# Optimization experiments

Measured on AMD Instinct MI355X. Metric: run time of the kernel, lower is better.

## Reference

```python
import jax, jax.numpy as jnp
import numpy as np

N_NODES = 100000
N_EDGES = 1600000
IN_CH, MID_CH, BOT_CH = 128, 128, 64


def setup_inputs() -> dict:
    key = jax.random.key(0)
    ks = jax.random.split(key, 10)
    x = jax.random.normal(ks[0], (N_NODES, IN_CH), dtype=jnp.float32)
    edge_index = jax.random.randint(ks[1], (2, N_EDGES), 0, N_NODES, dtype=jnp.int64)
    s = 0.05
    # GCNConv weights follow torch Linear convention: out = x @ W.T + b (bias added post-aggregation)
    W1 = jax.random.normal(ks[2], (MID_CH, IN_CH), dtype=jnp.float32) * s
    b1 = jnp.zeros((MID_CH,), dtype=jnp.float32)
    W2 = jax.random.normal(ks[3], (BOT_CH, MID_CH), dtype=jnp.float32) * s
    b2 = jnp.zeros((BOT_CH,), dtype=jnp.float32)
    W3 = jax.random.normal(ks[4], (MID_CH, BOT_CH), dtype=jnp.float32) * s
    b3 = jnp.zeros((MID_CH,), dtype=jnp.float32)
    W4 = jax.random.normal(ks[5], (IN_CH, MID_CH), dtype=jnp.float32) * s
    b4 = jnp.zeros((IN_CH,), dtype=jnp.float32)
    return {"x": x, "edge_index": edge_index,
            "W1": W1, "b1": b1, "W2": W2, "b2": b2,
            "W3": W3, "b3": b3, "W4": W4, "b4": b4}


def _gcn_conv(x, src, dst, norm, W, b, n):
    # linear transform first (small GEMM), then gather-normalize-scatter
    h = x @ W.T                                   # [N, out]
    msg = h[src] * norm[:, None]                  # [E+N, out] gathered messages
    out = jax.ops.segment_sum(msg, dst, num_segments=n)
    return out + b


def reference(x, edge_index, W1, b1, W2, b2, W3, b3, W4, b4):
    n = N_NODES
    # add self-loops (PyG GCNConv default)
    loop = jnp.arange(n, dtype=edge_index.dtype)
    src = jnp.concatenate([edge_index[0], loop])
    dst = jnp.concatenate([edge_index[1], loop])
    # symmetric degree normalization: deg includes self-loops -> deg >= 1
    deg = jax.ops.segment_sum(jnp.ones_like(dst, dtype=x.dtype), dst, num_segments=n)
    dinv = jax.lax.rsqrt(deg)
    norm = dinv[src] * dinv[dst]                  # [E+N]
    # encoder
    h = jax.nn.relu(_gcn_conv(x, src, dst, norm, W1, b1, n))
    z = _gcn_conv(h, src, dst, norm, W2, b2, n)
    # decoder
    h = jax.nn.relu(_gcn_conv(z, src, dst, norm, W3, b3, n))
    out = _gcn_conv(h, src, dst, norm, W4, b4, n)
    return out
```

## Files before the change

### kernel.cpp

```cpp
#include <hip/hip_runtime.h>

typedef unsigned int u32;
typedef unsigned short u16;
typedef short bf16x4 __attribute__((ext_vector_type(4)));
typedef short bf16x8 __attribute__((ext_vector_type(8)));
typedef float f32x4 __attribute__((ext_vector_type(4)));

__device__ inline u16 f2bf_rne(float f) {
    u32 b = __float_as_uint(f);
    return (u16)((b + 0x7FFFu + ((b >> 16) & 1u)) >> 16);
}
__device__ inline u32 packbf2(float lo, float hi) {
    return (u32)f2bf_rne(lo) | ((u32)f2bf_rne(hi) << 16);
}
__device__ inline float bf2f(u16 h) { return __uint_as_float((u32)h << 16); }
__device__ inline float2 bfpair(u32 q) {
    float2 f;
    f.x = __uint_as_float(q << 16);
    f.y = __uint_as_float(q & 0xFFFF0000u);
    return f;
}

__global__ void k_detect(const int* __restrict__ p, int n_int32, u32* __restrict__ flag) {
    __shared__ int s[256];
    int tid = threadIdx.x;
    int acc = 0;
    int limit = n_int32 < 2048 ? n_int32 : 2048;
    for (int i = 1 + 2 * tid; i < limit; i += 512) acc |= p[i];
    s[tid] = acc;
    __syncthreads();
    for (int o = 128; o > 0; o >>= 1) {
        if (tid < o) s[tid] |= s[tid + o];
        __syncthreads();
    }
    if (tid == 0) *flag = (s[0] == 0) ? 1u : 0u;
}

__global__ void k_convert(const void* __restrict__ p, int n, const u32* __restrict__ flag,
                          int* __restrict__ out) {
    int i = blockIdx.x * blockDim.x + threadIdx.x;
    if (i >= n) return;
    if (*flag) out[i] = (int)((const long long*)p)[i];
    else       out[i] = ((const int*)p)[i];
}

template <int CIN, int COUT>
__global__ void k_wpack(const float* __restrict__ W, u16* __restrict__ Wpk) {
    int i = blockIdx.x * 256 + threadIdx.x;
    if (i >= CIN * COUT) return;
    int o = i / CIN, k = i % CIN;
    int fi = o >> 4, l15 = o & 15;
    int ks = k >> 5, w = k & 31;
    int h = w >> 4, l4 = (w & 15) >> 2, off = w & 3;
    int lane = l4 * 16 + l15;
    int e = h * 4 + off;
    constexpr int KS = CIN / 32;
    Wpk[(size_t)(((fi * KS + ks) * 64 + lane) * 8 + e)] = f2bf_rne(W[i]);
}

__global__ void k_init(u32* __restrict__ deg, u32* __restrict__ cnt, int N) {
    int i = blockIdx.x * blockDim.x + threadIdx.x;
    if (i < N) { deg[i] = 1u; cnt[i] = 0u; }
}

__global__ __launch_bounds__(256) void k_count(const int* __restrict__ dst,
                                               u32* __restrict__ deg, int E, int N) {
    int xcd = blockIdx.x & 7;
    int sub = blockIdx.x >> 3;
    int nsub = gridDim.x >> 3;
    int lo = (int)((long long)N * xcd >> 3);
    int hi = (int)((long long)N * (xcd + 1) >> 3);
    for (int e = sub * 256 + threadIdx.x; e < E; e += nsub * 256) {
        int d = dst[e];
        if (d >= lo && d < hi) atomicAdd(&deg[d], 1u);
    }
}

__global__ void k_dinv(const u32* __restrict__ deg, float* __restrict__ dinv, int N) {
    int i = blockIdx.x * blockDim.x + threadIdx.x;
    if (i < N) dinv[i] = rsqrtf((float)deg[i]);
}

__global__ void k_scan_a(const u32* __restrict__ deg, u32* __restrict__ partial, int N) {
    __shared__ u32 s[256];
    int tid = threadIdx.x;
    int base = blockIdx.x * 1024 + tid * 4;
    u32 sum = 0;
#pragma unroll
    for (int j = 0; j < 4; ++j) {
        int v = base + j;
        sum += (v < N) ? (deg[v] - 1u) : 0u;
    }
    s[tid] = sum;
    __syncthreads();
    for (int o = 128; o > 0; o >>= 1) {
        if (tid < o) s[tid] += s[tid + o];
        __syncthreads();
    }
    if (tid == 0) partial[blockIdx.x] = s[0];
}

__global__ void k_scan_b(u32* __restrict__ partial, int NB, int* __restrict__ row_ptr, int N) {
    __shared__ u32 s[128];
    int tid = threadIdx.x;
    u32 v = (tid < NB) ? partial[tid] : 0u;
    s[tid] = v;
    __syncthreads();
    for (int off = 1; off < 128; off <<= 1) {
        u32 t = (tid >= off) ? s[tid - off] : 0u;
        __syncthreads();
        s[tid] += t;
        __syncthreads();
    }
    if (tid < NB) partial[tid] = s[tid] - v;
    if (tid == 127) row_ptr[N] = (int)s[127];
}

__global__ void k_scan_c(const u32* __restrict__ deg, const u32* __restrict__ partial,
                         int* __restrict__ row_ptr, int N) {
    __shared__ u32 s[256];
    int tid = threadIdx.x;
    int base = blockIdx.x * 1024 + tid * 4;
    u32 vals[4];
    u32 sum = 0;
#pragma unroll
    for (int j = 0; j < 4; ++j) {
        int v = base + j;
        vals[j] = (v < N) ? (deg[v] - 1u) : 0u;
        sum += vals[j];
    }
    s[tid] = sum;
    __syncthreads();
    for (int off = 1; off < 256; off <<= 1) {
        u32 t = (tid >= off) ? s[tid - off] : 0u;
        __syncthreads();
        s[tid] += t;
        __syncthreads();
    }
    u32 run = s[tid] - sum + partial[blockIdx.x];
#pragma unroll
    for (int j = 0; j < 4; ++j) {
        int v = base + j;
        if (v < N) row_ptr[v] = (int)run;
        run += vals[j];
    }
}

__global__ __launch_bounds__(256) void k_fill(const int* __restrict__ src,
                                              const int* __restrict__ dst,
                                              const int* __restrict__ row_ptr,
                                              u32* __restrict__ cnt,
                                              int* __restrict__ col, int E, int N) {
    int xcd = blockIdx.x & 7;
    int sub = blockIdx.x >> 3;
    int nsub = gridDim.x >> 3;
    int lo = (int)((long long)N * xcd >> 3);
    int hi = (int)((long long)N * (xcd + 1) >> 3);
    for (int e = sub * 256 + threadIdx.x; e < E; e += nsub * 256) {
        int d = dst[e];
        if (d >= lo && d < hi) {
            int pos = row_ptr[d] + (int)atomicAdd(&cnt[d], 1u);
            col[pos] = src[e];
        }
    }
}

template <int CIN, int COUT, int MODE, bool IN_F32>
__global__ __launch_bounds__(512, 4) void k_mgemm(const void* __restrict__ Xv,
                                                  const u16* __restrict__ Wpk,
                                                  const float* __restrict__ aux,
                                                  u16* __restrict__ Gout, int N,
                                                  int tiles, int tpb) {
    constexpr int PITCH = CIN + 8;
    constexpr int EPITCH = COUT + 8;
    constexpr int KS = CIN / 32;
    constexpr int NT = COUT / 32;
    constexpr int CHUNKS = COUT / 8;
    __shared__ __align__(16) u16 sX[64 * PITCH];
    __shared__ __align__(16) u16 sE[64 * EPITCH];

    int tid = threadIdx.x, wid = tid >> 6, lane = tid & 63;
    int l15 = lane & 15, l4 = lane >> 4;
    int rg = wid >> 1;
    int cg = wid & 1;

    bf16x8 wfrag[NT][KS];
#pragma unroll
    for (int nt = 0; nt < NT; ++nt) {
        int fi = cg * NT + nt;
#pragma unroll
        for (int ks = 0; ks < KS; ++ks)
            wfrag[nt][ks] = *(const bf16x8*)&Wpk[(size_t)(((fi * KS + ks) * 64 + lane) * 8)];
    }
    float bv[NT];
    if (MODE == 1) {
#pragma unroll
        for (int nt = 0; nt < NT; ++nt) bv[nt] = aux[cg * (COUT / 2) + nt * 16 + l15];
    }

    int t0 = blockIdx.x * tpb;
    int t1 = t0 + tpb; if (t1 > tiles) t1 = tiles;

    for (int t = t0; t < t1; ++t) {
        int rowbase = t * 64;

        if (IN_F32) {
            const float* Xf = (const float*)Xv;
            for (int i = tid * 8; i < 64 * CIN; i += 512 * 8) {
                int r = i / CIN, k = i % CIN;
                int row = rowbase + r;
                if (row >= N) row = N - 1;
                const float4* xp = (const float4*)(Xf + (size_t)row * CIN + k);
                float4 a = xp[0], b = xp[1];
                uint4 pk;
                pk.x = packbf2(a.x, a.y);
                pk.y = packbf2(a.z, a.w);
                pk.z = packbf2(b.x, b.y);
                pk.w = packbf2(b.z, b.w);
                *(uint4*)&sX[r * PITCH + k] = pk;
            }
        } else {
            const u16* Xb = (const u16*)Xv;
            for (int i = tid * 8; i < 64 * CIN; i += 512 * 8) {
                int r = i / CIN, k = i % CIN;
                int row = rowbase + r;
                if (row >= N) row = N - 1;
                *(bf16x8*)&sX[r * PITCH + k] = *(const bf16x8*)&Xb[(size_t)row * CIN + k];
            }
        }
        __syncthreads();

        f32x4 acc[NT];
#pragma unroll
        for (int nt = 0; nt < NT; ++nt) acc[nt] = (f32x4){0.f, 0.f, 0.f, 0.f};

        const u16* xrow = &sX[(rg * 16 + l15) * PITCH + 4 * l4];
#pragma unroll
        for (int ks = 0; ks < KS; ++ks) {
            bf16x4 a0 = *(const bf16x4*)(xrow + ks * 32);
            bf16x4 a1 = *(const bf16x4*)(xrow + ks * 32 + 16);
            bf16x8 av = __builtin_shufflevector(a0, a1, 0, 1, 2, 3, 4, 5, 6, 7);
#pragma unroll
            for (int nt = 0; nt < NT; ++nt)
                acc[nt] = __builtin_amdgcn_mfma_f32_16x16x32_bf16(av, wfrag[nt][ks], acc[nt], 0, 0, 0);
        }

#pragma unroll
        for (int i = 0; i < 4; ++i) {
            int rl = rg * 16 + 4 * l4 + i;
            int row = rowbase + rl;
            int rc = row < N ? row : N - 1;
            float s = (MODE == 0) ? aux[rc] : 0.f;
#pragma unroll
            for (int nt = 0; nt < NT; ++nt) {
                float a = acc[nt][i];
                float o = (MODE == 0) ? a * s : fmaxf(a + bv[nt], 0.f);
                sE[rl * EPITCH + cg * (COUT / 2) + nt * 16 + l15] = f2bf_rne(o);
            }
        }
        __syncthreads();

        for (int a = tid; a < 64 * CHUNKS; a += 512) {
            int rl = a / CHUNKS, ch = a % CHUNKS;
            int row = rowbase + rl;
            if (row < N)
                *(uint4*)&Gout[(size_t)row * COUT + ch * 8] =
                    *(const uint4*)&sE[rl * EPITCH + ch * 8];
        }
    }
}

template <bool OUT_BF16, bool RELU, bool HAS_BIAS>
__global__ __launch_bounds__(256) void k_spmm128(const u32* __restrict__ Gq,
                                                 const int* __restrict__ rp,
                                                 const int* __restrict__ col,
                                                 const float* __restrict__ dinv,
                                                 const float* __restrict__ bias,
                                                 void* __restrict__ Y, int N) {
    int wid = threadIdx.x >> 6, lane = threadIdx.x & 63;
    int v0 = blockIdx.x * 8 + wid * 2;
    if (v0 >= N) return;
    int v1 = v0 + 1;
    bool has1 = (v1 < N);

    float2 acc0 = bfpair(Gq[(size_t)v0 * 64 + lane]);
    int e0 = rp[v0], f0 = rp[v0 + 1];
    float2 acc1 = {0.f, 0.f};
    int e1 = 0, f1 = 0;
    if (has1) {
        acc1 = bfpair(Gq[(size_t)v1 * 64 + lane]);
        e1 = f0; f1 = rp[v1 + 1];
    }

    while (e0 + 8 <= f0 && e1 + 8 <= f1) {
        int u0[8], u1[8];
#pragma unroll
        for (int j = 0; j < 8; ++j) u0[j] = col[e0 + j];
#pragma unroll
        for (int j = 0; j < 8; ++j) u1[j] = col[e1 + j];
        u32 q0[8], q1[8];
#pragma unroll
        for (int j = 0; j < 8; ++j) q0[j] = Gq[(size_t)u0[j] * 64 + lane];
#pragma unroll
        for (int j = 0; j < 8; ++j) q1[j] = Gq[(size_t)u1[j] * 64 + lane];
#pragma unroll
        for (int j = 0; j < 8; ++j) {
            float2 a = bfpair(q0[j]);
            acc0.x += a.x; acc0.y += a.y;
        }
#pragma unroll
        for (int j = 0; j < 8; ++j) {
            float2 a = bfpair(q1[j]);
            acc1.x += a.x; acc1.y += a.y;
        }
        e0 += 8; e1 += 8;
    }
    for (; e0 + 8 <= f0; e0 += 8) {
        int u[8];
#pragma unroll
        for (int j = 0; j < 8; ++j) u[j] = col[e0 + j];
        u32 q[8];
#pragma unroll
        for (int j = 0; j < 8; ++j) q[j] = Gq[(size_t)u[j] * 64 + lane];
#pragma unroll
        for (int j = 0; j < 8; ++j) {
            float2 a = bfpair(q[j]);
            acc0.x += a.x; acc0.y += a.y;
        }
    }
    for (; e1 + 8 <= f1; e1 += 8) {
        int u[8];
#pragma unroll
        for (int j = 0; j < 8; ++j) u[j] = col[e1 + j];
        u32 q[8];
#pragma unroll
        for (int j = 0; j < 8; ++j) q[j] = Gq[(size_t)u[j] * 64 + lane];
#pragma unroll
        for (int j = 0; j < 8; ++j) {
            float2 a = bfpair(q[j]);
            acc1.x += a.x; acc1.y += a.y;
        }
    }
    for (; e0 < f0; ++e0) {
        float2 a = bfpair(Gq[(size_t)col[e0] * 64 + lane]);
        acc0.x += a.x; acc0.y += a.y;
    }
    for (; e1 < f1; ++e1) {
        float2 a = bfpair(Gq[(size_t)col[e1] * 64 + lane]);
        acc1.x += a.x; acc1.y += a.y;
    }

    {
        float s = dinv[v0];
        float rx = acc0.x * s, ry = acc0.y * s;
        if (HAS_BIAS) { rx += bias[2 * lane]; ry += bias[2 * lane + 1]; }
        if (RELU) { rx = fmaxf(rx, 0.f); ry = fmaxf(ry, 0.f); }
        if (OUT_BF16) ((u32*)Y)[(size_t)v0 * 64 + lane] = packbf2(rx, ry);
        else {
            float2 o2; o2.x = rx; o2.y = ry;
            *(float2*)((float*)Y + (size_t)v0 * 128 + 2 * lane) = o2;
        }
    }
    if (has1) {
        float s = dinv[v1];
        float rx = acc1.x * s, ry = acc1.y * s;
        if (HAS_BIAS) { rx += bias[2 * lane]; ry += bias[2 * lane + 1]; }
        if (RELU) { rx = fmaxf(rx, 0.f); ry = fmaxf(ry, 0.f); }
        if (OUT_BF16) ((u32*)Y)[(size_t)v1 * 64 + lane] = packbf2(rx, ry);
        else {
            float2 o2; o2.x = rx; o2.y = ry;
            *(float2*)((float*)Y + (size_t)v1 * 128 + 2 * lane) = o2;
        }
    }
}

template <bool OUT_BF16, bool RELU, bool HAS_BIAS, bool PRESCALE>
__global__ __launch_bounds__(256) void k_spmm64(const u16* __restrict__ G16,
                                                const int* __restrict__ rp,
                                                const int* __restrict__ col,
                                                const float* __restrict__ dinv,
                                                const float* __restrict__ bias,
                                                void* __restrict__ Y, int N) {
    int wid = threadIdx.x >> 6, lane = threadIdx.x & 63;
    int v0 = blockIdx.x * 8 + wid * 2;
    if (v0 >= N) return;
    int v1 = v0 + 1;
    bool has1 = (v1 < N);

    float acc0 = bf2f(G16[(size_t)v0 * 64 + lane]);
    int e0 = rp[v0], f0 = rp[v0 + 1];
    float acc1 = 0.f;
    int e1 = 0, f1 = 0;
    if (has1) {
        acc1 = bf2f(G16[(size_t)v1 * 64 + lane]);
        e1 = f0; f1 = rp[v1 + 1];
    }

    while (e0 + 8 <= f0 && e1 + 8 <= f1) {
        int u0[8], u1[8];
#pragma unroll
        for (int j = 0; j < 8; ++j) u0[j] = col[e0 + j];
#pragma unroll
        for (int j = 0; j < 8; ++j) u1[j] = col[e1 + j];
        u16 g0[8], g1[8];
#pragma unroll
        for (int j = 0; j < 8; ++j) g0[j] = G16[(size_t)u0[j] * 64 + lane];
#pragma unroll
        for (int j = 0; j < 8; ++j) g1[j] = G16[(size_t)u1[j] * 64 + lane];
        acc0 += ((bf2f(g0[0]) + bf2f(g0[1])) + (bf2f(g0[2]) + bf2f(g0[3]))) +
                ((bf2f(g0[4]) + bf2f(g0[5])) + (bf2f(g0[6]) + bf2f(g0[7])));
        acc1 += ((bf2f(g1[0]) + bf2f(g1[1])) + (bf2f(g1[2]) + bf2f(g1[3]))) +
                ((bf2f(g1[4]) + bf2f(g1[5])) + (bf2f(g1[6]) + bf2f(g1[7])));
        e0 += 8; e1 += 8;
    }
    for (; e0 + 8 <= f0; e0 += 8) {
        int u[8];
#pragma unroll
        for (int j = 0; j < 8; ++j) u[j] = col[e0 + j];
        u16 g[8];
#pragma unroll
        for (int j = 0; j < 8; ++j) g[j] = G16[(size_t)u[j] * 64 + lane];
        acc0 += ((bf2f(g[0]) + bf2f(g[1])) + (bf2f(g[2]) + bf2f(g[3]))) +
                ((bf2f(g[4]) + bf2f(g[5])) + (bf2f(g[6]) + bf2f(g[7])));
    }
    for (; e1 + 8 <= f1; e1 += 8) {
        int u[8];
#pragma unroll
        for (int j = 0; j < 8; ++j) u[j] = col[e1 + j];
        u16 g[8];
#pragma unroll
        for (int j = 0; j < 8; ++j) g[j] = G16[(size_t)u[j] * 64 + lane];
        acc1 += ((bf2f(g[0]) + bf2f(g[1])) + (bf2f(g[2]) + bf2f(g[3]))) +
                ((bf2f(g[4]) + bf2f(g[5])) + (bf2f(g[6]) + bf2f(g[7])));
    }
    for (; e0 < f0; ++e0) acc0 += bf2f(G16[(size_t)col[e0] * 64 + lane]);
    for (; e1 < f1; ++e1) acc1 += bf2f(G16[(size_t)col[e1] * 64 + lane]);

    {
        float s = dinv[v0];
        float r = acc0 * s;
        if (HAS_BIAS) r += bias[lane];
        if (RELU) r = fmaxf(r, 0.f);
        if (PRESCALE) r *= s;
        if (OUT_BF16) ((u16*)Y)[(size_t)v0 * 64 + lane] = f2bf_rne(r);
        else          ((float*)Y)[(size_t)v0 * 64 + lane] = r;
    }
    if (has1) {
        float s = dinv[v1];
        float r = acc1 * s;
        if (HAS_BIAS) r += bias[lane];
        if (RELU) r = fmaxf(r, 0.f);
        if (PRESCALE) r *= s;
        if (OUT_BF16) ((u16*)Y)[(size_t)v1 * 64 + lane] = f2bf_rne(r);
        else          ((float*)Y)[(size_t)v1 * 64 + lane] = r;
    }
}

extern "C" void kernel_launch(void* const* d_in, const int* in_sizes, int n_in,
                              void* d_out, int out_size, void* d_ws, size_t ws_size,
                              hipStream_t stream) {
    const float* x  = (const float*)d_in[0];
    const void*  ei = d_in[1];
    const float* W1 = (const float*)d_in[2];
    const float* b1 = (const float*)d_in[3];
    const float* W2 = (const float*)d_in[4];
    const float* b2 = (const float*)d_in[5];
    const float* W3 = (const float*)d_in[6];
    const float* b3 = (const float*)d_in[7];
    const float* W4 = (const float*)d_in[8];
    const float* b4 = (const float*)d_in[9];

    const int N = in_sizes[0] / 128;
    const int E = in_sizes[1] / 2;

    size_t off = 0;
    auto alloc = [&](size_t bytes) -> void* {
        void* p = (char*)d_ws + off;
        off += (bytes + 255) & ~(size_t)255;
        return p;
    };
    u32*   flag    = (u32*)  alloc(4);
    int*   src32   = (int*)  alloc((size_t)E * 4);
    int*   dst32   = (int*)  alloc((size_t)E * 4);
    u32*   deg     = (u32*)  alloc((size_t)N * 4);
    float* dinv    = (float*)alloc((size_t)N * 4);
    int*   row_ptr = (int*)  alloc((size_t)(N + 1) * 4);
    u32*   cnt     = (u32*)  alloc((size_t)N * 4);
    u32*   partial = (u32*)  alloc(256 * 4);
    int*   col     = (int*)  alloc((size_t)E * 4);
    u16*   Wp1     = (u16*)  alloc(128 * 128 * 2);
    u16*   Wp2     = (u16*)  alloc(64 * 128 * 2);
    u16*   Wp3     = (u16*)  alloc(128 * 64 * 2);
    u16*   Wp4     = (u16*)  alloc(128 * 128 * 2);
    u16*   BUF1    = (u16*)  alloc((size_t)N * 128 * 2);
    u16*   BUF2    = (u16*)  alloc((size_t)N * 128 * 2);
    u16*   BUF3    = (u16*)  alloc((size_t)N * 64 * 2);
    u16*   Zbf     = (u16*)d_out;

    const int n2 = 2 * E;
    const int NB = (N + 1023) / 1024;

    k_detect<<<1, 256, 0, stream>>>((const int*)ei, n2, flag);
    k_convert<<<(n2 + 255) / 256, 256, 0, stream>>>(ei, n2, flag, src32);
    int* dstp = src32 + E;
    k_init<<<(N + 255) / 256, 256, 0, stream>>>(deg, cnt, N);
    k_count<<<1024, 256, 0, stream>>>(dstp, deg, E, N);
    k_dinv<<<(N + 255) / 256, 256, 0, stream>>>(deg, dinv, N);
    k_scan_a<<<NB, 256, 0, stream>>>(deg, partial, N);
    k_scan_b<<<1, 128, 0, stream>>>(partial, NB, row_ptr, N);
    k_scan_c<<<NB, 256, 0, stream>>>(deg, partial, row_ptr, N);
    k_fill<<<1024, 256, 0, stream>>>(src32, dstp, row_ptr, cnt, col, E, N);
    (void)dst32;

    k_wpack<128, 128><<<(128 * 128 + 255) / 256, 256, 0, stream>>>(W1, Wp1);
    k_wpack<128, 64><<<(128 * 64 + 255) / 256, 256, 0, stream>>>(W2, Wp2);
    k_wpack<64, 128><<<(64 * 128 + 255) / 256, 256, 0, stream>>>(W3, Wp3);
    k_wpack<128, 128><<<(128 * 128 + 255) / 256, 256, 0, stream>>>(W4, Wp4);

    const int tiles = (N + 63) / 64;
    const int gM = tiles < 512 ? tiles : 512;
    const int tpb = (tiles + gM - 1) / gM;
    const int gS = (N + 7) / 8;

    k_mgemm<128, 128, 0, true><<<gM, 512, 0, stream>>>(x, Wp1, dinv, BUF1, N, tiles, tpb);
    k_spmm128<true, true, true><<<gS, 256, 0, stream>>>((const u32*)BUF1, row_ptr, col, dinv, b1, BUF2, N);

    k_mgemm<128, 64, 0, false><<<gM, 512, 0, stream>>>(BUF2, Wp2, dinv, BUF3, N, tiles, tpb);
    k_spmm64<true, false, true, true><<<gS, 256, 0, stream>>>(BUF3, row_ptr, col, dinv, b2, Zbf, N);

    k_spmm64<true, false, false, false><<<gS, 256, 0, stream>>>(Zbf, row_ptr, col, dinv, b2, BUF1, N);
    k_mgemm<64, 128, 1, false><<<gM, 512, 0, stream>>>(BUF1, Wp3, b3, BUF2, N, tiles, tpb);

    k_mgemm<128, 128, 0, false><<<gM, 512, 0, stream>>>(BUF2, Wp4, dinv, BUF1, N, tiles, tpb);
    k_spmm128<false, false, true><<<gS, 256, 0, stream>>>((const u32*)BUF1, row_ptr, col, dinv, b4, d_out, N);
}
```

Before: 490.2 us.

## Fuse decoder GEMMs, restructure 64-wide SpMM with half-wave edge split, add nontemporal loads

Layer-3 and layer-4 dense transforms are fused into one kernel that keeps the ReLU'd intermediate in shared memory, removing a global round trip of the 128-wide hidden activations. The 64-channel SpMM now processes one node per wave, with each half-wave handling alternate edges through 32-bit paired bf16 loads, then combines the halves with a cross-lane shuffle. Edge index loads and the final fp32 output stores use nontemporal hints to reduce cache pollution. The fused GEMM launches one block per tile, needs about 67KB of shared memory and has no persistent looping, which may limit occupancy.

Result: slower. 532.1 us (+8.5%).

```diff
diff --git a/kernel.cpp b/kernel.cpp
--- a/kernel.cpp
+++ b/kernel.cpp
@@ -5,6 +5,7 @@
 typedef short bf16x4 __attribute__((ext_vector_type(4)));
 typedef short bf16x8 __attribute__((ext_vector_type(8)));
 typedef float f32x4 __attribute__((ext_vector_type(4)));
+typedef float f32x2 __attribute__((ext_vector_type(2)));
 
 __device__ inline u16 f2bf_rne(float f) {
     u32 b = __float_as_uint(f);
@@ -270,6 +271,107 @@
     }
 }
 
+__global__ __launch_bounds__(512, 2) void k_mgemm34(const u16* __restrict__ Xb,
+                                                    const u16* __restrict__ Wp3,
+                                                    const u16* __restrict__ Wp4,
+                                                    const float* __restrict__ b3,
+                                                    const float* __restrict__ dinv,
+                                                    u16* __restrict__ Gout, int N) {
+    constexpr int P1 = 72;
+    constexpr int P2 = 136;
+    __shared__ __align__(16) u16 sW4[128 * 128];
+    __shared__ __align__(16) u16 sBuf[64 * P2];
+    __shared__ __align__(16) u16 sH[64 * P2];
+
+    int tid = threadIdx.x, wid = tid >> 6, lane = tid & 63;
+    int l15 = lane & 15, l4 = lane >> 4;
+    int rg = wid >> 1, cg = wid & 1;
+    int rowbase = blockIdx.x * 64;
+
+    bf16x8 wf3[4][2];
+#pragma unroll
+    for (int nt = 0; nt < 4; ++nt) {
+        int fi = cg * 4 + nt;
+#pragma unroll
+        for (int ks = 0; ks < 2; ++ks)
+            wf3[nt][ks] = *(const bf16x8*)&Wp3[(size_t)(((fi * 2 + ks) * 64 + lane) * 8)];
+    }
+    float bv[4];
+#pragma unroll
+    for (int nt = 0; nt < 4; ++nt) bv[nt] = b3[cg * 64 + nt * 16 + l15];
+
+    for (int i = tid * 8; i < 128 * 128; i += 512 * 8)
+        *(bf16x8*)&sW4[i] = *(const bf16x8*)&Wp4[i];
+
+    for (int i = tid * 8; i < 64 * 64; i += 512 * 8) {
+        int r = i / 64, k = i % 64;
+        int row = rowbase + r;
+        if (row >= N) row = N - 1;
+        *(bf16x8*)&sBuf[r * P1 + k] = *(const bf16x8*)&Xb[(size_t)row * 64 + k];
+    }
+    __syncthreads();
+
+    f32x4 acc[4];
+#pragma unroll
+    for (int nt = 0; nt < 4; ++nt) acc[nt] = (f32x4){0.f, 0.f, 0.f, 0.f};
+    {
+        const u16* xrow = &sBuf[(rg * 16 + l15) * P1 + 4 * l4];
+#pragma unroll
+        for (int ks = 0; ks < 2; ++ks) {
+            bf16x4 a0 = *(const bf16x4*)(xrow + ks * 32);
+            bf16x4 a1 = *(const bf16x4*)(xrow + ks * 32 + 16);
+            bf16x8 av = __builtin_shufflevector(a0, a1, 0, 1, 2, 3, 4, 5, 6, 7);
+#pragma unroll
+            for (int nt = 0; nt < 4; ++nt)
+                acc[nt] = __builtin_amdgcn_mfma_f32_16x16x32_bf16(av, wf3[nt][ks], acc[nt], 0, 0, 0);
+        }
+    }
+#pragma unroll
+    for (int i = 0; i < 4; ++i) {
+        int rl = rg * 16 + 4 * l4 + i;
+#pragma unroll
+        for (int nt = 0; nt < 4; ++nt)
+            sH[rl * P2 + cg * 64 + nt * 16 + l15] = f2bf_rne(fmaxf(acc[nt][i] + bv[nt], 0.f));
+    }
+    __syncthreads();
+
+#pragma unroll
+    for (int nt = 0; nt < 4; ++nt) acc[nt] = (f32x4){0.f, 0.f, 0.f, 0.f};
+    {
+        const u16* xrow = &sH[(rg * 16 + l15) * P2 + 4 * l4];
+#pragma unroll
+        for (int ks = 0; ks < 4; ++ks) {
+            bf16x4 a0 = *(const bf16x4*)(xrow + ks * 32);
+            bf16x4 a1 = *(const bf16x4*)(xrow + ks * 32 + 16);
+            bf16x8 av = __builtin_shufflevector(a0, a1, 0, 1, 2, 3, 4, 5, 6, 7);
+#pragma unroll
+            for (int nt = 0; nt < 4; ++nt) {
+                int fi = cg * 4 + nt;
+                bf16x8 bw = *(const bf16x8*)&sW4[(size_t)(((fi * 4 + ks) * 64 + lane) * 8)];
+                acc[nt] = __builtin_amdgcn_mfma_f32_16x16x32_bf16(av, bw, acc[nt], 0, 0, 0);
+            }
+        }
+    }
+#pragma unroll
+    for (int i = 0; i < 4; ++i) {
+        int rl = rg * 16 + 4 * l4 + i;
+        int row = rowbase + rl;
+        int rc = row < N ? row : N - 1;
+        float s = dinv[rc];
+#pragma unroll
+        for (int nt = 0; nt < 4; ++nt)
+            sBuf[rl * P2 + cg * 64 + nt * 16 + l15] = f2bf_rne(acc[nt][i] * s);
+    }
+    __syncthreads();
+
+    for (int a = tid; a < 64 * 16; a += 512) {
+        int rl = a / 16, ch = a % 16;
+        int row = rowbase + rl;
+        if (row < N)
+            *(uint4*)&Gout[(size_t)row * 128 + ch * 8] = *(const uint4*)&sBuf[rl * P2 + ch * 8];
+    }
+}
+
 template <bool OUT_BF16, bool RELU, bool HAS_BIAS>
 __global__ __launch_bounds__(256) void k_spmm128(const u32* __restrict__ Gq,
                                                  const int* __restrict__ rp,
@@ -295,9 +397,9 @@
     while (e0 + 8 <= f0 && e1 + 8 <= f1) {
         int u0[8], u1[8];
 #pragma unroll
-        for (int j = 0; j < 8; ++j) u0[j] = col[e0 + j];
-#pragma unroll
-        for (int j = 0; j < 8; ++j) u1[j] = col[e1 + j];
+        for (int j = 0; j < 8; ++j) u0[j] = __builtin_nontemporal_load(&col[e0 + j]);
+#pragma unroll
+        for (int j = 0; j < 8; ++j) u1[j] = __builtin_nontemporal_load(&col[e1 + j]);
         u32 q0[8], q1[8];
 #pragma unroll
         for (int j = 0; j < 8; ++j) q0[j] = Gq[(size_t)u0[j] * 64 + lane];
@@ -318,7 +420,7 @@
     for (; e0 + 8 <= f0; e0 += 8) {
         int u[8];
 #pragma unroll
-        for (int j = 0; j < 8; ++j) u[j] = col[e0 + j];
+        for (int j = 0; j < 8; ++j) u[j] = __builtin_nontemporal_load(&col[e0 + j]);
         u32 q[8];
 #pragma unroll
         for (int j = 0; j < 8; ++j) q[j] = Gq[(size_t)u[j] * 64 + lane];
@@ -331,7 +433,7 @@
     for (; e1 + 8 <= f1; e1 += 8) {
         int u[8];
 #pragma unroll
-        for (int j = 0; j < 8; ++j) u[j] = col[e1 + j];
+        for (int j = 0; j < 8; ++j) u[j] = __builtin_nontemporal_load(&col[e1 + j]);
         u32 q[8];
 #pragma unroll
         for (int j = 0; j < 8; ++j) q[j] = Gq[(size_t)u[j] * 64 + lane];
@@ -357,8 +459,8 @@
         if (RELU) { rx = fmaxf(rx, 0.f); ry = fmaxf(ry, 0.f); }
         if (OUT_BF16) ((u32*)Y)[(size_t)v0 * 64 + lane] = packbf2(rx, ry);
         else {
-            float2 o2; o2.x = rx; o2.y = ry;
-            *(float2*)((float*)Y + (size_t)v0 * 128 + 2 * lane) = o2;
+            f32x2 o2 = {rx, ry};
+            __builtin_nontemporal_store(o2, (f32x2*)((float*)Y + (size_t)v0 * 128 + 2 * lane));
         }
     }
     if (has1) {
@@ -368,8 +470,8 @@
         if (RELU) { rx = fmaxf(rx, 0.f); ry = fmaxf(ry, 0.f); }
         if (OUT_BF16) ((u32*)Y)[(size_t)v1 * 64 + lane] = packbf2(rx, ry);
         else {
-            float2 o2; o2.x = rx; o2.y = ry;
-            *(float2*)((float*)Y + (size_t)v1 * 128 + 2 * lane) = o2;
+            f32x2 o2 = {rx, ry};
+            __builtin_nontemporal_store(o2, (f32x2*)((float*)Y + (size_t)v1 * 128 + 2 * lane));
         }
     }
 }
@@ -382,77 +484,53 @@
                                                 const float* __restrict__ bias,
                                                 void* __restrict__ Y, int N) {
     int wid = threadIdx.x >> 6, lane = threadIdx.x & 63;
-    int v0 = blockIdx.x * 8 + wid * 2;
-    if (v0 >= N) return;
-    int v1 = v0 + 1;
-    bool has1 = (v1 < N);
-
-    float acc0 = bf2f(G16[(size_t)v0 * 64 + lane]);
-    int e0 = rp[v0], f0 = rp[v0 + 1];
-    float acc1 = 0.f;
-    int e1 = 0, f1 = 0;
-    if (has1) {
-        acc1 = bf2f(G16[(size_t)v1 * 64 + lane]);
-        e1 = f0; f1 = rp[v1 + 1];
-    }
-
-    while (e0 + 8 <= f0 && e1 + 8 <= f1) {
-        int u0[8], u1[8];
-#pragma unroll
-        for (int j = 0; j < 8; ++j) u0[j] = col[e0 + j];
-#pragma unroll
-        for (int j = 0; j < 8; ++j) u1[j] = col[e1 + j];
-        u16 g0[8], g1[8];
-#pragma unroll
-        for (int j = 0; j < 8; ++j) g0[j] = G16[(size_t)u0[j] * 64 + lane];
-#pragma unroll
-        for (int j = 0; j < 8; ++j) g1[j] = G16[(size_t)u1[j] * 64 + lane];
-        acc0 += ((bf2f(g0[0]) + bf2f(g0[1])) + (bf2f(g0[2]) + bf2f(g0[3]))) +
-                ((bf2f(g0[4]) + bf2f(g0[5])) + (bf2f(g0[6]) + bf2f(g0[7])));
-        acc1 += ((bf2f(g1[0]) + bf2f(g1[1])) + (bf2f(g1[2]) + bf2f(g1[3]))) +
-                ((bf2f(g1[4]) + bf2f(g1[5])) + (bf2f(g1[6]) + bf2f(g1[7])));
-        e0 += 8; e1 += 8;
-    }
-    for (; e0 + 8 <= f0; e0 += 8) {
+    int v = blockIdx.x * 4 + wid;
+    if (v >= N) return;
+    int l31 = lane & 31, h = lane >> 5;
+    const u32* Gq = (const u32*)G16;
+
+    float2 acc = {0.f, 0.f};
+    if (h == 0) acc = bfpair(Gq[(size_t)v * 32 + l31]);
+
+    int e = rp[v], end = rp[v + 1];
+    for (; e + 16 <= end; e += 16) {
         int u[8];
 #pragma unroll
-        for (int j = 0; j < 8; ++j) u[j] = col[e0 + j];
-        u16 g[8];
-#pragma unroll
-        for (int j = 0; j < 8; ++j) g[j] = G16[(size_t)u[j] * 64 + lane];
-        acc0 += ((bf2f(g[0]) + bf2f(g[1])) + (bf2f(g[2]) + bf2f(g[3]))) +
-                ((bf2f(g[4]) + bf2f(g[5])) + (bf2f(g[6]) + bf2f(g[7])));
-    }
-    for (; e1 + 8 <= f1; e1 += 8) {
-        int u[8];
-#pragma unroll
-        for (int j = 0; j < 8; ++j) u[j] = col[e1 + j];
-        u16 g[8];
-#pragma unroll
-        for (int j = 0; j < 8; ++j) g[j] = G16[(size_t)u[j] * 64 + lane];
-        acc1 += ((bf2f(g[0]) + bf2f(g[1])) + (bf2f(g[2]) + bf2f(g[3]))) +
-                ((bf2f(g[4]) + bf2f(g[5])) + (bf2f(g[6]) + bf2f(g[7])));
-    }
-    for (; e0 < f0; ++e0) acc0 += bf2f(G16[(size_t)col[e0] * 64 + lane]);
-    for (; e1 < f1; ++e1) acc1 += bf2f(G16[(size_t)col[e1] * 64 + lane]);
-
-    {
-        float s = dinv[v0];
-        float r = acc0 * s;
-        if (HAS_BIAS) r += bias[lane];
-        if (RELU) r = fmaxf(r, 0.f);
-        if (PRESCALE) r *= s;
-        if (OUT_BF16) ((u16*)Y)[(size_t)v0 * 64 + lane] = f2bf_rne(r);
-        else          ((float*)Y)[(size_t)v0 * 64 + lane] = r;
-    }
-    if (has1) {
-        float s = dinv[v1];
-        float r = acc1 * s;
-        if (HAS_BIAS) r += bias[lane];
-        if (RELU) r = fmaxf(r, 0.f);
-        if (PRESCALE) r *= s;
-        if (OUT_BF16) ((u16*)Y)[(size_t)v1 * 64 + lane] = f2bf_rne(r);
-        else          ((float*)Y)[(size_t)v1 * 64 + lane] = r;
+        for (int j = 0; j < 8; ++j) u[j] = __builtin_nontemporal_load(&col[e + 2 * j + h]);
+        u32 q[8];
+#pragma unroll
+        for (int j = 0; j < 8; ++j) q[j] = Gq[(size_t)u[j] * 32 + l31];
+#pragma unroll
+        for (int j = 0; j < 8; ++j) {
+            float2 a = bfpair(q[j]);
+            acc.x += a.x; acc.y += a.y;
+        }
+    }
+    for (; e + 2 <= end; e += 2) {
+        int u = __builtin_nontemporal_load(&col[e + h]);
+        float2 a = bfpair(Gq[(size_t)u * 32 + l31]);
+        acc.x += a.x; acc.y += a.y;
+    }
+    if (e < end && h == 0) {
+        float2 a = bfpair(Gq[(size_t)col[e] * 32 + l31]);
+        acc.x += a.x; acc.y += a.y;
+    }
+
+    acc.x += __shfl_xor(acc.x, 32);
+    acc.y += __shfl_xor(acc.y, 32);
+
+    if (h == 0) {
+        float s = dinv[v];
+        float rx = acc.x * s, ry = acc.y * s;
+        if (HAS_BIAS) { rx += bias[2 * l31]; ry += bias[2 * l31 + 1]; }
+        if (RELU) { rx = fmaxf(rx, 0.f); ry = fmaxf(ry, 0.f); }
+        if (PRESCALE) { rx *= s; ry *= s; }
+        if (OUT_BF16) {
+            ((u32*)Y)[(size_t)v * 32 + l31] = packbf2(rx, ry);
+        } else {
+            float2 o2; o2.x = rx; o2.y = ry;
+            *(float2*)((float*)Y + (size_t)v * 64 + 2 * l31) = o2;
+        }
     }
 }
 
@@ -480,8 +558,7 @@
         return p;
     };
     u32*   flag    = (u32*)  alloc(4);
-    int*   src32   = (int*)  alloc((size_t)E * 4);
-    int*   dst32   = (int*)  alloc((size_t)E * 4);
+    int*   src32   = (int*)  alloc((size_t)E * 2 * 4);
     u32*   deg     = (u32*)  alloc((size_t)N * 4);
     float* dinv    = (float*)alloc((size_t)N * 4);
     int*   row_ptr = (int*)  alloc((size_t)(N + 1) * 4);
@@ -510,7 +587,6 @@
     k_scan_b<<<1, 128, 0, stream>>>(partial, NB, row_ptr, N);
     k_scan_c<<<NB, 256, 0, stream>>>(deg, partial, row_ptr, N);
     k_fill<<<1024, 256, 0, stream>>>(src32, dstp, row_ptr, cnt, col, E, N);
-    (void)dst32;
 
     k_wpack<128, 128><<<(128 * 128 + 255) / 256, 256, 0, stream>>>(W1, Wp1);
     k_wpack<128, 64><<<(128 * 64 + 255) / 256, 256, 0, stream>>>(W2, Wp2);
@@ -521,16 +597,17 @@
     const int gM = tiles < 512 ? tiles : 512;
     const int tpb = (tiles + gM - 1) / gM;
     const int gS = (N + 7) / 8;
+    const int gS1 = (N + 3) / 4;
 
     k_mgemm<128, 128, 0, true><<<gM, 512, 0, stream>>>(x, Wp1, dinv, BUF1, N, tiles, tpb);
     k_spmm128<true, true, true><<<gS, 256, 0, stream>>>((const u32*)BUF1, row_ptr, col, dinv, b1, BUF2, N);
 
     k_mgemm<128, 64, 0, false><<<gM, 512, 0, stream>>>(BUF2, Wp2, dinv, BUF3, N, tiles, tpb);
-    k_spmm64<true, false, true, true><<<gS, 256, 0, stream>>>(BUF3, row_ptr, col, dinv, b2, Zbf, N);
-
-    k_spmm64<true, false, false, false><<<gS, 256, 0, stream>>>(Zbf, row_ptr, col, dinv, b2, BUF1, N);
-    k_mgemm<64, 128, 1, false><<<gM, 512, 0, stream>>>(BUF1, Wp3, b3, BUF2, N, tiles, tpb);
-
-    k_mgemm<128, 128, 0, false><<<gM, 512, 0, stream>>>(BUF2, Wp4, dinv, BUF1, N, tiles, tpb);
-    k_spmm128<false, false, true><<<gS, 256, 0, stream>>>((const u32*)BUF1, row_ptr, col, dinv, b4, d_out, N);
-}
+    k_spmm64<true, false, true, true><<<gS1, 256, 0, stream>>>(BUF3, row_ptr, col, dinv, b2, Zbf, N);
+
+    k_spmm64<true, false, false, false><<<gS1, 256, 0, stream>>>(Zbf, row_ptr, col, dinv, b2, BUF1, N);
+
+    k_mgemm34<<<tiles, 512, 0, stream>>>(BUF1, Wp3, Wp4, b3, dinv, BUF2, N);
+
+    k_spmm128<false, false, true><<<gS, 256, 0, stream>>>((const u32*)BUF2, row_ptr, col, dinv, b4, d_out, N);
+}
```

## Pre-bucket edges by destination octant before degree count and CSR fill

Applied to the files above, without the earlier changes.

Replaces the int64-to-int32 conversion plus the two full-edge passes, each of which filtered edges by XCD range, with one bucketing kernel. That kernel reads the raw edge list once and groups (dst, src) pairs into eight per-octant global buffers using shared-memory staging. The count and fill kernels then read only their own octant's bucket, which removes the 8x redundant reads of the dst array. It adds a shared-memory staging kernel with global atomics. Each bucket is capped at E/4 entries, so a skewed destination distribution would silently drop edges.

New measurement: 533.5 us. +8.8%, slower.

```diff
diff --git a/kernel.cpp b/kernel.cpp
--- a/kernel.cpp
+++ b/kernel.cpp
@@ -34,14 +34,6 @@
         __syncthreads();
     }
     if (tid == 0) *flag = (s[0] == 0) ? 1u : 0u;
-}
-
-__global__ void k_convert(const void* __restrict__ p, int n, const u32* __restrict__ flag,
-                          int* __restrict__ out) {
-    int i = blockIdx.x * blockDim.x + threadIdx.x;
-    if (i >= n) return;
-    if (*flag) out[i] = (int)((const long long*)p)[i];
-    else       out[i] = ((const int*)p)[i];
 }
 
 template <int CIN, int COUT>
@@ -58,21 +50,104 @@
     Wpk[(size_t)(((fi * KS + ks) * 64 + lane) * 8 + e)] = f2bf_rne(W[i]);
 }
 
-__global__ void k_init(u32* __restrict__ deg, u32* __restrict__ cnt, int N) {
+__global__ void k_init(u32* __restrict__ deg, u32* __restrict__ cnt,
+                       u32* __restrict__ gcnt, int N) {
     int i = blockIdx.x * blockDim.x + threadIdx.x;
     if (i < N) { deg[i] = 1u; cnt[i] = 0u; }
-}
-
-__global__ __launch_bounds__(256) void k_count(const int* __restrict__ dst,
-                                               u32* __restrict__ deg, int E, int N) {
-    int xcd = blockIdx.x & 7;
-    int sub = blockIdx.x >> 3;
-    int nsub = gridDim.x >> 3;
-    int lo = (int)((long long)N * xcd >> 3);
-    int hi = (int)((long long)N * (xcd + 1) >> 3);
-    for (int e = sub * 256 + threadIdx.x; e < E; e += nsub * 256) {
-        int d = dst[e];
-        if (d >= lo && d < hi) atomicAdd(&deg[d], 1u);
+    if (blockIdx.x == 0 && threadIdx.x < 8) gcnt[threadIdx.x] = 0u;
+}
+
+__global__ __launch_bounds__(256) void k_bucket(const void* __restrict__ ei, int E, int N,
+                                                const u32* __restrict__ flag,
+                                                int2* __restrict__ gbuf, int bst,
+                                                u32* __restrict__ gcnt) {
+    __shared__ int2 sbuf[8][512];
+    __shared__ u32 scnt[8];
+    __shared__ u32 sbase[8];
+    int tid = threadIdx.x;
+    if (tid < 8) scnt[tid] = 0u;
+    __syncthreads();
+    bool is64 = (*flag != 0u);
+    const long long* p64 = (const long long*)ei;
+    const int* p32 = (const int*)ei;
+    long long NN = N;
+
+    for (int base = blockIdx.x * 256; base < E; base += gridDim.x * 256) {
+        int e = base + tid;
+        if (e < E) {
+            int s, d;
+            if (is64) { s = (int)p64[e]; d = (int)p64[E + e]; }
+            else      { s = p32[e];      d = p32[E + e]; }
+            int oct = (int)((8LL * d) / NN);
+            u32 slot = atomicAdd(&scnt[oct], 1u);
+            if (slot < 512u) { int2 en; en.x = d; en.y = s; sbuf[oct][slot] = en; }
+        }
+        __syncthreads();
+        if (tid < 8) {
+            u32 c = scnt[tid]; u32 nf = c & ~255u;
+            sbase[tid] = nf ? atomicAdd(&gcnt[tid], nf) : 0u;
+        }
+        __syncthreads();
+#pragma unroll
+        for (int oct = 0; oct < 8; ++oct) {
+            u32 c = scnt[oct]; u32 nf = c & ~255u;
+            if (nf) {
+                u32 b = sbase[oct];
+                for (u32 i = tid; i < nf; i += 256) {
+                    u32 pos = b + i;
+                    if (pos < (u32)bst) gbuf[(size_t)oct * bst + pos] = sbuf[oct][i];
+                }
+            }
+        }
+        __syncthreads();
+#pragma unroll
+        for (int oct = 0; oct < 8; ++oct) {
+            u32 c = scnt[oct]; u32 nf = c & ~255u;
+            u32 rem = c - nf;
+            if (nf && tid < rem) sbuf[oct][tid] = sbuf[oct][nf + tid];
+        }
+        __syncthreads();
+        if (tid < 8) scnt[tid] &= 255u;
+        __syncthreads();
+    }
+    if (tid < 8) {
+        u32 c = scnt[tid];
+        sbase[tid] = c ? atomicAdd(&gcnt[tid], c) : 0u;
+    }
+    __syncthreads();
+#pragma unroll
+    for (int oct = 0; oct < 8; ++oct) {
+        u32 c = scnt[oct];
+        u32 b = sbase[oct];
+        for (u32 i = tid; i < c; i += 256) {
+            u32 pos = b + i;
+            if (pos < (u32)bst) gbuf[(size_t)oct * bst + pos] = sbuf[oct][i];
+        }
+    }
+}
+
+__global__ __launch_bounds__(256) void k_bcount(const int2* __restrict__ gbuf, int bst,
+                                                const u32* __restrict__ gcnt,
+                                                u32* __restrict__ deg) {
+    int g = blockIdx.x & 7, sub = blockIdx.x >> 3, nsub = gridDim.x >> 3;
+    u32 n = gcnt[g]; if (n > (u32)bst) n = (u32)bst;
+    const int2* b = gbuf + (size_t)g * bst;
+    for (u32 i = sub * 256 + threadIdx.x; i < n; i += nsub * 256)
+        atomicAdd(&deg[b[i].x], 1u);
+}
+
+__global__ __launch_bounds__(256) void k_bfill(const int2* __restrict__ gbuf, int bst,
+                                               const u32* __restrict__ gcnt,
+                                               const int* __restrict__ row_ptr,
+                                               u32* __restrict__ cnt,
+                                               int* __restrict__ col) {
+    int g = blockIdx.x & 7, sub = blockIdx.x >> 3, nsub = gridDim.x >> 3;
+    u32 n = gcnt[g]; if (n > (u32)bst) n = (u32)bst;
+    const int2* b = gbuf + (size_t)g * bst;
+    for (u32 i = sub * 256 + threadIdx.x; i < n; i += nsub * 256) {
+        int2 en = b[i];
+        int pos = row_ptr[en.x] + (int)atomicAdd(&cnt[en.x], 1u);
+        col[pos] = en.y;
     }
 }
 
@@ -143,25 +218,6 @@
         int v = base + j;
         if (v < N) row_ptr[v] = (int)run;
         run += vals[j];
-    }
-}
-
-__global__ __launch_bounds__(256) void k_fill(const int* __restrict__ src,
-                                              const int* __restrict__ dst,
-                                              const int* __restrict__ row_ptr,
-                                              u32* __restrict__ cnt,
-                                              int* __restrict__ col, int E, int N) {
-    int xcd = blockIdx.x & 7;
-    int sub = blockIdx.x >> 3;
-    int nsub = gridDim.x >> 3;
-    int lo = (int)((long long)N * xcd >> 3);
-    int hi = (int)((long long)N * (xcd + 1) >> 3);
-    for (int e = sub * 256 + threadIdx.x; e < E; e += nsub * 256) {
-        int d = dst[e];
-        if (d >= lo && d < hi) {
-            int pos = row_ptr[d] + (int)atomicAdd(&cnt[d], 1u);
-            col[pos] = src[e];
-        }
     }
 }
 
@@ -472,6 +528,7 @@
 
     const int N = in_sizes[0] / 128;
     const int E = in_sizes[1] / 2;
+    const int BST = E / 4;
 
     size_t off = 0;
     auto alloc = [&](size_t bytes) -> void* {
@@ -480,14 +537,14 @@
         return p;
     };
     u32*   flag    = (u32*)  alloc(4);
-    int*   src32   = (int*)  alloc((size_t)E * 4);
-    int*   dst32   = (int*)  alloc((size_t)E * 4);
     u32*   deg     = (u32*)  alloc((size_t)N * 4);
     float* dinv    = (float*)alloc((size_t)N * 4);
     int*   row_ptr = (int*)  alloc((size_t)(N + 1) * 4);
     u32*   cnt     = (u32*)  alloc((size_t)N * 4);
     u32*   partial = (u32*)  alloc(256 * 4);
+    u32*   gcnt    = (u32*)  alloc(8 * 4);
     int*   col     = (int*)  alloc((size_t)E * 4);
+    int2*  gbuf    = (int2*) alloc((size_t)8 * BST * 8);
     u16*   Wp1     = (u16*)  alloc(128 * 128 * 2);
     u16*   Wp2     = (u16*)  alloc(64 * 128 * 2);
     u16*   Wp3     = (u16*)  alloc(128 * 64 * 2);
@@ -501,16 +558,14 @@
     const int NB = (N + 1023) / 1024;
 
     k_detect<<<1, 256, 0, stream>>>((const int*)ei, n2, flag);
-    k_convert<<<(n2 + 255) / 256, 256, 0, stream>>>(ei, n2, flag, src32);
-    int* dstp = src32 + E;
-    k_init<<<(N + 255) / 256, 256, 0, stream>>>(deg, cnt, N);
-    k_count<<<1024, 256, 0, stream>>>(dstp, deg, E, N);
+    k_init<<<(N + 255) / 256, 256, 0, stream>>>(deg, cnt, gcnt, N);
+    k_bucket<<<256, 256, 0, stream>>>(ei, E, N, flag, gbuf, BST, gcnt);
+    k_bcount<<<1024, 256, 0, stream>>>(gbuf, BST, gcnt, deg);
     k_dinv<<<(N + 255) / 256, 256, 0, stream>>>(deg, dinv, N);
     k_scan_a<<<NB, 256, 0, stream>>>(deg, partial, N);
     k_scan_b<<<1, 128, 0, stream>>>(partial, NB, row_ptr, N);
     k_scan_c<<<NB, 256, 0, stream>>>(deg, partial, row_ptr, N);
-    k_fill<<<1024, 256, 0, stream>>>(src32, dstp, row_ptr, cnt, col, E, N);
-    (void)dst32;
+    k_bfill<<<1024, 256, 0, stream>>>(gbuf, BST, gcnt, row_ptr, cnt, col);
 
     k_wpack<128, 128><<<(128 * 128 + 255) / 256, 256, 0, stream>>>(W1, Wp1);
     k_wpack<128, 64><<<(128 * 64 + 255) / 256, 256, 0, stream>>>(W2, Wp2);
@@ -529,6 +584,7 @@
     k_spmm64<true, false, true, true><<<gS, 256, 0, stream>>>(BUF3, row_ptr, col, dinv, b2, Zbf, N);
 
     k_spmm64<true, false, false, false><<<gS, 256, 0, stream>>>(Zbf, row_ptr, col, dinv, b2, BUF1, N);
+
     k_mgemm<64, 128, 1, false><<<gM, 512, 0, stream>>>(BUF1, Wp3, b3, BUF2, N, tiles, tpb);
 
     k_mgemm<128, 128, 0, false><<<gM, 512, 0, stream>>>(BUF2, Wp4, dinv, BUF1, N, tiles, tpb);
```
